# Kernel tuning notes

Hardware: AMD Instinct MI355X
Metric: run time of the kernel (lower is better)

The kernel has to match this reference:

```python
import jax, jax.numpy as jnp
import numpy as np

BITS = 4
BLOCK_SIZE = 64
EPS = 1e-8


def nf_table():
    # NormalFloat table: inverse normal CDF at midpoints, normalized to [-1, 1].
    n_levels = 2 ** BITS
    p = (jnp.arange(n_levels, dtype=jnp.float32) + 0.5) / n_levels
    q = jax.scipy.special.ndtri(p)
    q = q / jnp.max(jnp.abs(q))
    return q.astype(jnp.float16)  # original stores table in fp16


def setup_inputs() -> dict:
    key = jax.random.key(0)
    x = jax.random.normal(key, (2048, 8192, 1), dtype=jnp.float32)
    return {"x": x}


def reference(x):
    table = nf_table()                          # (16,) fp16
    orig_shape = x.shape                        # (R, C, 1)
    R, C = orig_shape[0], orig_shape[1]
    nb = C // BLOCK_SIZE
    xb = x.reshape(R, nb, BLOCK_SIZE)           # (R, nb, bs)

    # --- compress ---
    x_min = jnp.min(xb, axis=2, keepdims=True)  # (R, nb, 1)
    x_max = jnp.max(xb, axis=2, keepdims=True)
    scales = jnp.squeeze(x_max - x_min, -1)     # (R, nb)
    x_norm = 2.0 * (xb - x_min) / (x_max - x_min + EPS) - 1.0
    # distance to each of 16 codebook levels, argmin over last axis
    dist = jnp.abs(x_norm[..., None] - table.astype(x_norm.dtype))  # (R, nb, bs, 16)
    q_idx = jnp.argmin(dist, axis=-1)           # (R, nb, bs) int

    # double quantization of scales (8-bit over each row)
    s_min = jnp.min(scales, axis=-1, keepdims=True)   # (R, 1)
    s_max = jnp.max(scales, axis=-1, keepdims=True)
    scales_q = jnp.round((scales - s_min) / (s_max - s_min + EPS) * 255.0)  # (R, nb)

    # --- decompress ---
    scales_rec = s_min + scales_q / 255.0 * (s_max - s_min)   # (R, nb)
    scales_rec = scales_rec[..., None]                        # (R, nb, 1)
    w_block = table[q_idx].astype(jnp.float32)                # (R, nb, bs)
    w_block = (w_block + 1.0) / 2.0 * scales_rec + x_min
    return w_block.reshape(orig_shape)
```

## Files before the change

kernel.cpp:

```cpp
#include <hip/hip_runtime.h>
#include <cmath>

#define C_COLS 8192

struct NfArgs {
    float tbl[16];
    float kexp;
};

__global__ __launch_bounds__(256) void nf4_main_kernel(
        const float* __restrict__ x, float* __restrict__ out, NfArgs args) {
#pragma clang fp contract(off)
    __shared__ float stbl[16];
    __shared__ float smin[4], smax[4];

    const int row  = blockIdx.x;
    const int wave = threadIdx.x >> 6;
    const int lane = threadIdx.x & 63;
    const long base = (long)row * C_COLS + (long)wave * 2048;
    const float4* __restrict__ xin4 = reinterpret_cast<const float4*>(x + base);
    float4* __restrict__ out4       = reinterpret_cast<float4*>(out + base);

    float4 v[8];
#pragma unroll
    for (int k = 0; k < 8; ++k) v[k] = xin4[k * 64 + lane];

    if (threadIdx.x < 16) stbl[threadIdx.x] = args.tbl[threadIdx.x];

    float bmin[8], bmax[8], srec[8];
    float tmin = 3.4e38f, tmax = -3.4e38f;
#pragma unroll
    for (int k = 0; k < 8; ++k) {
        float m = fminf(fminf(v[k].x, v[k].y), fminf(v[k].z, v[k].w));
        float M = fmaxf(fmaxf(v[k].x, v[k].y), fmaxf(v[k].z, v[k].w));
#pragma unroll
        for (int off = 1; off < 16; off <<= 1) {
            m = fminf(m, __shfl_xor(m, off));
            M = fmaxf(M, __shfl_xor(M, off));
        }
        bmin[k] = m;
        bmax[k] = M;
        float sc = M - m;
        tmin = fminf(tmin, sc);
        tmax = fmaxf(tmax, sc);
    }
    tmin = fminf(tmin, __shfl_xor(tmin, 16));
    tmin = fminf(tmin, __shfl_xor(tmin, 32));
    tmax = fmaxf(tmax, __shfl_xor(tmax, 16));
    tmax = fmaxf(tmax, __shfl_xor(tmax, 32));

    if (lane == 0) { smin[wave] = tmin; smax[wave] = tmax; }
    __syncthreads();

    const float s_min  = fminf(fminf(smin[0], smin[1]), fminf(smin[2], smin[3]));
    const float s_max  = fmaxf(fmaxf(smax[0], smax[1]), fmaxf(smax[2], smax[3]));
    const float srange = s_max - s_min;
    const float sden   = srange + 1e-8f;
    const float sqr    = 1.0f / sden;

#pragma unroll
    for (int k = 0; k < 8; ++k) {
        float sc = bmax[k] - bmin[k];
        float sq = rintf(((sc - s_min) * sqr) * 255.0f);
        srec[k]  = s_min + sq / 255.0f * srange;
    }

    const float kexp = args.kexp;
#pragma unroll
    for (int k = 0; k < 8; ++k) {
        const float bm  = bmin[k];
        const float den = (bmax[k] - bm) + 1e-8f;
        const float s2r = 2.0f / den;
        const float sr  = srec[k];
        float xv[4] = { v[k].x, v[k].y, v[k].z, v[k].w };
        float wv[4];
#pragma unroll
        for (int c = 0; c < 4; ++c) {
            float p  = (xv[c] - bm) * s2r;
            float xn = p - 1.0f;
            float eb = __builtin_amdgcn_exp2f(xn * kexp);
            float f  = 16.0f * __builtin_amdgcn_rcpf(1.0f + eb);
            int ci = (int)f;
            ci = min(max(ci, 1), 14);
            float tm1 = stbl[ci - 1];
            float tc  = stbl[ci];
            float tp1 = stbl[ci + 1];
            float a0 = fabsf(xn - tm1);
            float a1 = fabsf(xn - tc);
            float a2 = fabsf(xn - tp1);
            float t01  = (a1 < a0) ? tc : tm1;
            float amin = fminf(a1, a0);
            float tsel = (a2 < amin) ? tp1 : t01;
            wv[c] = (tsel + 1.0f) * 0.5f * sr + bm;
        }
        float4 r; r.x = wv[0]; r.y = wv[1]; r.z = wv[2]; r.w = wv[3];
        out4[k * 64 + lane] = r;
    }
}

static void compute_nf_args(NfArgs* a) {
    double z[16];
    for (int i = 0; i < 16; ++i) {
        double p  = (2.0 * i + 1.0) / 32.0;
        double pl = (p < 0.5) ? p : 1.0 - p;
        double t  = std::sqrt(-2.0 * std::log(pl));
        double zz = t - (2.30753 + 0.27061 * t) / (1.0 + t * (0.99229 + 0.04481 * t));
        if (p < 0.5) zz = -zz;
        for (int it = 0; it < 3; ++it) {
            double Phi = 0.5 * std::erfc(-zz * 0.7071067811865476);
            double phi = 0.3989422804014326779 * std::exp(-0.5 * zz * zz);
            zz -= (Phi - p) / phi;
        }
        z[i] = zz;
    }
    float zf[16], qmax = 0.0f;
    for (int i = 0; i < 16; ++i) { zf[i] = (float)z[i]; qmax = std::fmax(qmax, std::fabs(zf[i])); }
    for (int i = 0; i < 16; ++i) {
        float qn = zf[i] / qmax;
        double av = std::fabs((double)qn);
        int e; std::frexp(av, &e);
        double ulp = std::ldexp(1.0, e - 11);
        a->tbl[i] = (float)std::copysign(std::rint(av / ulp) * ulp, (double)qn);
    }
    a->kexp = (float)(-1.702 * 1.4426950408889634 * (double)qmax);
}

extern "C" void kernel_launch(void* const* d_in, const int* in_sizes, int n_in,
                              void* d_out, int out_size, void* d_ws, size_t ws_size,
                              hipStream_t stream) {
    const float* x = (const float*)d_in[0];
    float* out     = (float*)d_out;
    const int rows = in_sizes[0] / C_COLS;

    NfArgs args;
    compute_nf_args(&args);

    nf4_main_kernel<<<rows, 256, 0, stream>>>(x, out, args);
}
```

Measured before the change: 112.4 us.

## Remap each block to two lanes and pack table neighbors into float4

Each lane now loads 8 contiguous float4s (32 floats), so a 64-element quantization block spans only two adjacent lanes. The per-block min/max then needs one shuffle instead of four per k, and each lane keeps a single min/max/scale instead of eight. Codebook neighbors (i-1, i, i+1) are packed into a float4 in LDS, so each element does one 16-byte LDS read instead of three scalar reads. The cost is that global accesses are no longer coalesced across lanes, since each lane's 128-byte chunk is strided from its neighbors, which may hurt memory efficiency.

```diff
diff --git a/kernel.cpp b/kernel.cpp
--- a/kernel.cpp
+++ b/kernel.cpp
@@ -11,44 +11,49 @@
 __global__ __launch_bounds__(256) void nf4_main_kernel(
         const float* __restrict__ x, float* __restrict__ out, NfArgs args) {
 #pragma clang fp contract(off)
-    __shared__ float stbl[16];
-    __shared__ float smin[4], smax[4];
+    __shared__ float4 qtbl[16];
+    __shared__ float  smin[4], smax[4];
 
-    const int row  = blockIdx.x;
     const int wave = threadIdx.x >> 6;
     const int lane = threadIdx.x & 63;
-    const long base = (long)row * C_COLS + (long)wave * 2048;
-    const float4* __restrict__ xin4 = reinterpret_cast<const float4*>(x + base);
-    float4* __restrict__ out4       = reinterpret_cast<float4*>(out + base);
+    const long base = (long)blockIdx.x * C_COLS + (long)wave * 2048;
+    const float4* __restrict__ xin4 = reinterpret_cast<const float4*>(x + base) + lane * 8;
+    float4* __restrict__ out4       = reinterpret_cast<float4*>(out + base) + lane * 8;
 
     float4 v[8];
 #pragma unroll
-    for (int k = 0; k < 8; ++k) v[k] = xin4[k * 64 + lane];
+    for (int k = 0; k < 8; ++k) v[k] = xin4[k];
 
-    if (threadIdx.x < 16) stbl[threadIdx.x] = args.tbl[threadIdx.x];
+    if (threadIdx.x < 16) {
+        const int i = threadIdx.x;
+        float4 q;
+        q.x = args.tbl[(i > 0) ? i - 1 : 0];
+        q.y = args.tbl[i];
+        q.z = args.tbl[(i < 15) ? i + 1 : 15];
+        q.w = 0.0f;
+        qtbl[i] = q;
+    }
 
-    float bmin[8], bmax[8], srec[8];
-    float tmin = 3.4e38f, tmax = -3.4e38f;
+    float m4[8], M4[8];
 #pragma unroll
     for (int k = 0; k < 8; ++k) {
-        float m = fminf(fminf(v[k].x, v[k].y), fminf(v[k].z, v[k].w));
-        float M = fmaxf(fmaxf(v[k].x, v[k].y), fmaxf(v[k].z, v[k].w));
+        m4[k] = fminf(fminf(v[k].x, v[k].y), fminf(v[k].z, v[k].w));
+        M4[k] = fmaxf(fmaxf(v[k].x, v[k].y), fmaxf(v[k].z, v[k].w));
+    }
+    float m = m4[0], M = M4[0];
 #pragma unroll
-        for (int off = 1; off < 16; off <<= 1) {
-            m = fminf(m, __shfl_xor(m, off));
-            M = fmaxf(M, __shfl_xor(M, off));
-        }
-        bmin[k] = m;
-        bmax[k] = M;
-        float sc = M - m;
-        tmin = fminf(tmin, sc);
-        tmax = fmaxf(tmax, sc);
+    for (int k = 1; k < 8; ++k) { m = fminf(m, m4[k]); M = fmaxf(M, M4[k]); }
+    m = fminf(m, __shfl_xor(m, 1));
+    M = fmaxf(M, __shfl_xor(M, 1));
+    const float bm_blk = m, bM_blk = M;
+    const float sc     = bM_blk - bm_blk;
+
+    float tmin = sc, tmax = sc;
+#pragma unroll
+    for (int off = 2; off < 64; off <<= 1) {
+        tmin = fminf(tmin, __shfl_xor(tmin, off));
+        tmax = fmaxf(tmax, __shfl_xor(tmax, off));
     }
-    tmin = fminf(tmin, __shfl_xor(tmin, 16));
-    tmin = fminf(tmin, __shfl_xor(tmin, 32));
-    tmax = fmaxf(tmax, __shfl_xor(tmax, 16));
-    tmax = fmaxf(tmax, __shfl_xor(tmax, 32));
-
     if (lane == 0) { smin[wave] = tmin; smax[wave] = tmax; }
     __syncthreads();
 
@@ -58,43 +63,35 @@
     const float sden   = srange + 1e-8f;
     const float sqr    = 1.0f / sden;
 
+    const float sq   = rintf(((sc - s_min) * sqr) * 255.0f);
+    const float sr   = s_min + sq / 255.0f * srange;
+    const float den  = (bM_blk - bm_blk) + 1e-8f;
+    const float s2r  = 2.0f / den;
+    const float kexp = args.kexp;
+
 #pragma unroll
     for (int k = 0; k < 8; ++k) {
-        float sc = bmax[k] - bmin[k];
-        float sq = rintf(((sc - s_min) * sqr) * 255.0f);
-        srec[k]  = s_min + sq / 255.0f * srange;
-    }
-
-    const float kexp = args.kexp;
-#pragma unroll
-    for (int k = 0; k < 8; ++k) {
-        const float bm  = bmin[k];
-        const float den = (bmax[k] - bm) + 1e-8f;
-        const float s2r = 2.0f / den;
-        const float sr  = srec[k];
         float xv[4] = { v[k].x, v[k].y, v[k].z, v[k].w };
         float wv[4];
 #pragma unroll
         for (int c = 0; c < 4; ++c) {
-            float p  = (xv[c] - bm) * s2r;
+            float p  = (xv[c] - bm_blk) * s2r;
             float xn = p - 1.0f;
             float eb = __builtin_amdgcn_exp2f(xn * kexp);
             float f  = 16.0f * __builtin_amdgcn_rcpf(1.0f + eb);
             int ci = (int)f;
             ci = min(max(ci, 1), 14);
-            float tm1 = stbl[ci - 1];
-            float tc  = stbl[ci];
-            float tp1 = stbl[ci + 1];
-            float a0 = fabsf(xn - tm1);
-            float a1 = fabsf(xn - tc);
-            float a2 = fabsf(xn - tp1);
-            float t01  = (a1 < a0) ? tc : tm1;
+            float4 w3 = qtbl[ci];
+            float a0 = fabsf(xn - w3.x);
+            float a1 = fabsf(xn - w3.y);
+            float a2 = fabsf(xn - w3.z);
+            float t01  = (a1 < a0) ? w3.y : w3.x;
             float amin = fminf(a1, a0);
-            float tsel = (a2 < amin) ? tp1 : t01;
-            wv[c] = (tsel + 1.0f) * 0.5f * sr + bm;
+            float tsel = (a2 < amin) ? w3.z : t01;
+            wv[c] = (tsel + 1.0f) * 0.5f * sr + bm_blk;
         }
         float4 r; r.x = wv[0]; r.y = wv[1]; r.z = wv[2]; r.w = wv[3];
-        out4[k * 64 + lane] = r;
+        out4[k] = r;
     }
 }
 
```

New measurement: 121.7 us. 1.08x slower.
